# Optimization experiments

Hardware: AMD Instinct MI355X
Metric: run time of the kernel (lower is better)

## Reference

```python
import jax, jax.numpy as jnp
import numpy as np

HEAD_NUM = 8
NEG_BIG = 1e9  # additive mask constant from the original layer


def setup_inputs() -> dict:
    key = jax.random.key(0)
    ks = jax.random.split(key, 7)
    B, S, D = 4, 2048, 512
    return {
        "x": jax.random.normal(ks[0], (B, S, D), dtype=jnp.float32),
        "Wk": jax.random.normal(ks[1], (D, D), dtype=jnp.float32) * (1.0 / np.sqrt(D)),
        "bk": jax.random.normal(ks[2], (D,), dtype=jnp.float32) * 0.02,
        "Wv": jax.random.normal(ks[3], (D, D), dtype=jnp.float32) * (1.0 / np.sqrt(D)),
        "bv": jax.random.normal(ks[4], (D,), dtype=jnp.float32) * 0.02,
        "Wo": jax.random.normal(ks[5], (D, D), dtype=jnp.float32) * (1.0 / np.sqrt(D)),
        "bo": jax.random.normal(ks[6], (D,), dtype=jnp.float32) * 0.02,
    }


def reference(x, Wk, bk, Wv, bv, Wo, bo):
    B, S, D = x.shape
    H = HEAD_NUM
    hd = D // H
    # Original layer: query is NOT projected; key/value are.
    q = x
    k = x @ Wk + bk
    v = x @ Wv + bv
    # split heads: [B, H, S, hd]
    qh = q.reshape(B, S, H, hd).transpose(0, 2, 1, 3)
    kh = k.reshape(B, S, H, hd).transpose(0, 2, 1, 3)
    vh = v.reshape(B, S, H, hd).transpose(0, 2, 1, 3)
    # scaled dot-product scores [B, H, S, S] (normalized=True => 1/sqrt(head_dim))
    scale = 1.0 / jnp.sqrt(jnp.asarray(hd, dtype=x.dtype))
    e = jnp.einsum("bhqd,bhkd->bhqk", qh, kh) * scale
    # history_only=True => causal additive mask
    causal = jnp.tril(jnp.ones((S, S), dtype=x.dtype))
    e = e - (1.0 - causal) * NEG_BIG
    a = jax.nn.softmax(e, axis=-1)
    out = jnp.einsum("bhqk,bhkd->bhqd", a, vh)  # [B, H, S, hd]
    out = out.transpose(0, 2, 1, 3).reshape(B, S, D)
    return out @ Wo + bo
```

## Files before the change

### kernel.cpp

```cpp
#include <hip/hip_runtime.h>
#include <stdint.h>
#include <stddef.h>

typedef short bf16x8 __attribute__((ext_vector_type(8)));
typedef float f32x4 __attribute__((ext_vector_type(4)));
typedef int i32x4 __attribute__((ext_vector_type(4)));

#define AS1 __attribute__((address_space(1)))
#define AS3 __attribute__((address_space(3)))

#define KSCALE 0.18033688011112042f
#define MFMA16(A, B, C) __builtin_amdgcn_mfma_f32_16x16x32_bf16(A, B, C, 0, 0, 0)

__device__ __forceinline__ unsigned short f2bf(float f) {
    union { float f; uint32_t u; } v; v.f = f;
    return (unsigned short)((v.u + 0x7fffu + ((v.u >> 16) & 1u)) >> 16);
}

__global__ void cvt_f32_bf16(const float* __restrict__ in, unsigned short* __restrict__ out, int n4) {
    int i = blockIdx.x * blockDim.x + threadIdx.x;
    if (i >= n4) return;
    float4 v = reinterpret_cast<const float4*>(in)[i];
    ushort4 o;
    o.x = f2bf(v.x); o.y = f2bf(v.y); o.z = f2bf(v.z); o.w = f2bf(v.w);
    reinterpret_cast<ushort4*>(out)[i] = o;
}

__global__ void wtrans3(const float* __restrict__ Wk, const float* __restrict__ Wv,
                        const float* __restrict__ Wo,
                        unsigned short* __restrict__ WkT, unsigned short* __restrict__ WvT,
                        unsigned short* __restrict__ WoT) {
    __shared__ float tile[32][33];
    const float* W = (blockIdx.z == 0) ? Wk : (blockIdx.z == 1) ? Wv : Wo;
    unsigned short* WT = (blockIdx.z == 0) ? WkT : (blockIdx.z == 1) ? WvT : WoT;
    int bk = blockIdx.x * 32, bn = blockIdx.y * 32;
    int tx = threadIdx.x, ty = threadIdx.y;
#pragma unroll
    for (int r = 0; r < 32; r += 8)
        tile[ty + r][tx] = W[(size_t)(bk + ty + r) * 512 + bn + tx];
    __syncthreads();
#pragma unroll
    for (int r = 0; r < 32; r += 8)
        WT[(size_t)(bn + ty + r) * 512 + bk + tx] = f2bf(tile[tx][ty + r]);
}

template<int EPI>
__global__ __launch_bounds__(256, 2) void gemm64(const unsigned short* __restrict__ A,
                                                 const unsigned short* __restrict__ BT,
                                                 const float* __restrict__ bias,
                                                 void* __restrict__ outp) {
    __shared__ unsigned short lA[64 * 64];
    __shared__ unsigned short lB[128 * 64];
    const int tid = threadIdx.x;
    const int tile_n = blockIdx.x * 128;
    const int tile_m = blockIdx.y * 64;
    const int wid = tid >> 6, lane = tid & 63;
    const int wm = (wid >> 1) * 32, wn = (wid & 1) * 64;
    const int l16 = lane & 15, lg = lane >> 4;

    f32x4 acc[2][4];
#pragma unroll
    for (int i = 0; i < 2; ++i)
#pragma unroll
        for (int j = 0; j < 4; ++j)
            acc[i][j] = (f32x4){0.f, 0.f, 0.f, 0.f};

    const int r0 = tid >> 3;
    const int cr = tid & 7;

    for (int kt = 0; kt < 512; kt += 64) {
#pragma unroll
        for (int i = 0; i < 2; ++i) {
            int r = r0 + i * 32;
            int crs = cr ^ (r & 7);
            __builtin_amdgcn_global_load_lds((const AS1 void*)(A + (size_t)(tile_m + r) * 512 + kt + crs * 8),
                                             (AS3 void*)(&lA[(i * 256 + tid) * 8]), 16, 0, 0);
        }
#pragma unroll
        for (int i = 0; i < 4; ++i) {
            int r = r0 + i * 32;
            int crs = cr ^ (r & 7);
            __builtin_amdgcn_global_load_lds((const AS1 void*)(BT + (size_t)(tile_n + r) * 512 + kt + crs * 8),
                                             (AS3 void*)(&lB[(i * 256 + tid) * 8]), 16, 0, 0);
        }
        __syncthreads();
#pragma unroll
        for (int ks = 0; ks < 2; ++ks) {
            bf16x8 af[2], bfr[4];
#pragma unroll
            for (int f = 0; f < 2; ++f) {
                int ra = wm + f * 16 + l16;
                af[f] = *reinterpret_cast<const bf16x8*>(
                    reinterpret_cast<const char*>(lA) + ra * 128 + (((ks * 4 + lg) ^ (ra & 7)) << 4));
            }
#pragma unroll
            for (int f = 0; f < 4; ++f) {
                int rb = wn + f * 16 + l16;
                bfr[f] = *reinterpret_cast<const bf16x8*>(
                    reinterpret_cast<const char*>(lB) + rb * 128 + (((ks * 4 + lg) ^ (rb & 7)) << 4));
            }
#pragma unroll
            for (int fm = 0; fm < 2; ++fm)
#pragma unroll
                for (int fn = 0; fn < 4; ++fn)
                    acc[fm][fn] = MFMA16(af[fm], bfr[fn], acc[fm][fn]);
        }
        __syncthreads();
    }

#pragma unroll
    for (int fm = 0; fm < 2; ++fm)
#pragma unroll
        for (int fn = 0; fn < 4; ++fn) {
            int gm0 = tile_m + wm + fm * 16 + lg * 4;
            int gn = tile_n + wn + fn * 16 + l16;
            float bs = bias[gn];
#pragma unroll
            for (int r = 0; r < 4; ++r) {
                float v = acc[fm][fn][r] + bs;
                int m = gm0 + r;
                if (EPI == 0) {
                    v *= KSCALE;
                    int b = m >> 11, s = m & 2047, h = gn >> 6, d = gn & 63;
                    ((unsigned short*)outp)[(((size_t)(b * 8 + h) * 2048 + s) << 6) + d] = f2bf(v);
                } else if (EPI == 1) {
                    int b = m >> 11, s = m & 2047, h = gn >> 6, d = gn & 63;
                    ((unsigned short*)outp)[(((size_t)(b * 8 + h) * 64 + d) << 11) + s] = f2bf(v);
                } else {
                    ((float*)outp)[(size_t)m * 512 + gn] = v;
                }
            }
        }
}

__global__ __launch_bounds__(256, 3) void attn_f(const unsigned short* __restrict__ xq,
                                                 const unsigned short* __restrict__ kg,
                                                 const unsigned short* __restrict__ vT,
                                                 unsigned short* __restrict__ ob) {
    __shared__ unsigned short lsK[3][4096];
    __shared__ unsigned short lsV[3][4096];

    const int tid = threadIdx.x;
    const int lane = tid & 63;
    const int w = tid >> 6;
    const int l16 = lane & 15, lg = lane >> 4;
    const int bh = blockIdx.x, b = bh >> 3, h = bh & 7;
    const int qblk = 31 - blockIdx.y;
    const int qlo = qblk * 64 + w * 16;
    const int q = qlo + l16;

    const unsigned short* Kb = kg + (size_t)bh * (2048 * 64);
    const unsigned short* Vb = vT + (size_t)bh * (64 * 2048);

    const unsigned short* qp = xq + ((size_t)(b * 2048 + qlo + l16) * 512) + h * 64 + lg * 8;
    bf16x8 qf0 = *(const bf16x8*)qp;
    bf16x8 qf1 = *(const bf16x8*)(qp + 32);

    f32x4 o[4];
#pragma unroll
    for (int i = 0; i < 4; ++i) o[i] = (f32x4){0.f, 0.f, 0.f, 0.f};
    float lsum = 0.f;

    const int nph = qblk + 1;

    const int srow = tid >> 3;
    const int scs = (tid & 7) ^ (srow & 7);
    const int skey = 8 * ((srow >> 2) & 3) + (srow & 3) + 4 * (srow >> 4);

#define STAGE(B, PH) { \
        const int kv0_ = (PH) << 6; \
        __builtin_amdgcn_global_load_lds((const AS1 void*)(Kb + (size_t)(kv0_ + skey) * 64 + scs * 8), \
            (AS3 void*)(&lsK[B][(size_t)tid * 8]), 16, 0, 0); \
        __builtin_amdgcn_global_load_lds((const AS1 void*)(Kb + (size_t)(kv0_ + 32 + skey) * 64 + scs * 8), \
            (AS3 void*)(&lsK[B][(size_t)(256 + tid) * 8]), 16, 0, 0); \
        __builtin_amdgcn_global_load_lds((const AS1 void*)(Vb + (size_t)srow * 2048 + kv0_ + scs * 8), \
            (AS3 void*)(&lsV[B][(size_t)tid * 8]), 16, 0, 0); \
        __builtin_amdgcn_global_load_lds((const AS1 void*)(Vb + (size_t)(srow + 32) * 2048 + kv0_ + scs * 8), \
            (AS3 void*)(&lsV[B][(size_t)(256 + tid) * 8]), 16, 0, 0); }

#define QKGRP(G, PA, PB, KS, KVB) { \
            const char* r0p = (KS) + (32 * (G) + l16) * 128; \
            const char* r1p = r0p + 16 * 128; \
            bf16x8 k00 = *(const bf16x8*)(r0p + ((lg ^ sw) << 4)); \
            bf16x8 k01 = *(const bf16x8*)(r0p + (((lg + 4) ^ sw) << 4)); \
            bf16x8 k10 = *(const bf16x8*)(r1p + ((lg ^ sw) << 4)); \
            bf16x8 k11 = *(const bf16x8*)(r1p + (((lg + 4) ^ sw) << 4)); \
            f32x4 sA = (f32x4){0.f,0.f,0.f,0.f}, sB = (f32x4){0.f,0.f,0.f,0.f}; \
            __builtin_amdgcn_s_setprio(1); \
            sA = MFMA16(k00, qf0, sA); \
            sA = MFMA16(k01, qf1, sA); \
            sB = MFMA16(k10, qf0, sB); \
            sB = MFMA16(k11, qf1, sB); \
            __builtin_amdgcn_s_setprio(0); \
            if ((KVB) + 32 * (G) + 31 > qlo) { \
                _Pragma("unroll") \
                for (int r = 0; r < 4; ++r) { \
                    int kidx = (KVB) + 32 * (G) + 8 * lg + r; \
                    PA[r] = __builtin_amdgcn_exp2f(kidx > q ? -1e30f : sA[r]); \
                    PB[r] = __builtin_amdgcn_exp2f(kidx + 4 > q ? -1e30f : sB[r]); \
                } \
            } else { \
                _Pragma("unroll") \
                for (int r = 0; r < 4; ++r) { \
                    PA[r] = __builtin_amdgcn_exp2f(sA[r]); \
                    PB[r] = __builtin_amdgcn_exp2f(sB[r]); \
                } \
            } }

    const int sw = l16 & 7;
    STAGE(0, 0);
    if (nph > 1) STAGE(1, 1);
    int cur = 0, st = 2;
    for (int ph = 0; ph < nph; ++ph) {
        if (ph + 2 < nph) {
            STAGE(st, ph + 2);
            asm volatile("s_waitcnt vmcnt(8)" ::: "memory");
        } else if (ph + 1 < nph) {
            asm volatile("s_waitcnt vmcnt(4)" ::: "memory");
        } else {
            asm volatile("s_waitcnt vmcnt(0)" ::: "memory");
        }
        __builtin_amdgcn_s_barrier();
        asm volatile("" ::: "memory");
        {
            const char* KS = (const char*)lsK[cur];
            const char* VS = (const char*)lsV[cur];
            const int kvb = ph << 6;
            float pA0[4], pB0[4], pA1[4], pB1[4];
            QKGRP(0, pA0, pB0, KS, kvb)
            QKGRP(1, pA1, pB1, KS, kvb)
            lsum += ((pA0[0] + pA0[1]) + (pA0[2] + pA0[3]))
                  + ((pB0[0] + pB0[1]) + (pB0[2] + pB0[3]))
                  + ((pA1[0] + pA1[1]) + (pA1[2] + pA1[3]))
                  + ((pB1[0] + pB1[1]) + (pB1[2] + pB1[3]));
            uint32_t u0, u1, u2, u3, u4, u5, u6, u7;
            asm("v_cvt_pk_bf16_f32 %0, %1, %2" : "=v"(u0) : "v"(pA0[0]), "v"(pA0[1]));
            asm("v_cvt_pk_bf16_f32 %0, %1, %2" : "=v"(u1) : "v"(pA0[2]), "v"(pA0[3]));
            asm("v_cvt_pk_bf16_f32 %0, %1, %2" : "=v"(u2) : "v"(pB0[0]), "v"(pB0[1]));
            asm("v_cvt_pk_bf16_f32 %0, %1, %2" : "=v"(u3) : "v"(pB0[2]), "v"(pB0[3]));
            asm("v_cvt_pk_bf16_f32 %0, %1, %2" : "=v"(u4) : "v"(pA1[0]), "v"(pA1[1]));
            asm("v_cvt_pk_bf16_f32 %0, %1, %2" : "=v"(u5) : "v"(pA1[2]), "v"(pA1[3]));
            asm("v_cvt_pk_bf16_f32 %0, %1, %2" : "=v"(u6) : "v"(pB1[0]), "v"(pB1[1]));
            asm("v_cvt_pk_bf16_f32 %0, %1, %2" : "=v"(u7) : "v"(pB1[2]), "v"(pB1[3]));
            union { i32x4 i; bf16x8 h; } pu0, pu1;
            pu0.i = (i32x4){(int)u0, (int)u1, (int)u2, (int)u3};
            pu1.i = (i32x4){(int)u4, (int)u5, (int)u6, (int)u7};
            __builtin_amdgcn_s_setprio(1);
#pragma unroll
            for (int nb = 0; nb < 4; ++nb) {
                const char* vr = VS + (nb * 16 + l16) * 128;
                bf16x8 vf0 = *(const bf16x8*)(vr + ((lg ^ sw) << 4));
                bf16x8 vf1 = *(const bf16x8*)(vr + (((lg + 4) ^ sw) << 4));
                o[nb] = MFMA16(pu0.h, vf0, o[nb]);
                o[nb] = MFMA16(pu1.h, vf1, o[nb]);
            }
            __builtin_amdgcn_s_setprio(0);
        }
        asm volatile("" ::: "memory");
        __builtin_amdgcn_s_barrier();
        cur = (cur == 2) ? 0 : cur + 1;
        st = (st == 2) ? 0 : st + 1;
    }
#undef STAGE
#undef QKGRP

    lsum += __shfl_xor(lsum, 16, 64);
    lsum += __shfl_xor(lsum, 32, 64);
    float linv[4];
#pragma unroll
    for (int r = 0; r < 4; ++r)
        linv[r] = 1.f / __shfl(lsum, 4 * lg + r, 64);
#pragma unroll
    for (int nb = 0; nb < 4; ++nb)
#pragma unroll
        for (int r = 0; r < 4; ++r) {
            int s = qlo + 4 * lg + r;
            ob[(size_t)(b * 2048 + s) * 512 + h * 64 + nb * 16 + l16] = f2bf(o[nb][r] * linv[r]);
        }
}

extern "C" void kernel_launch(void* const* d_in, const int* in_sizes, int n_in,
                              void* d_out, int out_size, void* d_ws, size_t ws_size,
                              hipStream_t stream) {
    const float* x  = (const float*)d_in[0];
    const float* Wk = (const float*)d_in[1];
    const float* bk = (const float*)d_in[2];
    const float* Wv = (const float*)d_in[3];
    const float* bv = (const float*)d_in[4];
    const float* Wo = (const float*)d_in[5];
    const float* bo = (const float*)d_in[6];

    char* ws = (char*)d_ws;
    unsigned short* xb   = (unsigned short*)(ws);
    unsigned short* kbuf = (unsigned short*)(ws + (8ull << 20));
    unsigned short* vTb  = (unsigned short*)(ws + (16ull << 20));
    unsigned short* obuf = (unsigned short*)(ws + (24ull << 20));
    unsigned short* WkT  = (unsigned short*)(ws + (32ull << 20));
    unsigned short* WvT  = (unsigned short*)(ws + (33ull << 20));
    unsigned short* WoT  = (unsigned short*)(ws + (34ull << 20));

    cvt_f32_bf16<<<4096, 256, 0, stream>>>(x, xb, 1048576);
    wtrans3<<<dim3(16, 16, 3), dim3(32, 8), 0, stream>>>(Wk, Wv, Wo, WkT, WvT, WoT);

    dim3 gg(4, 128);
    gemm64<0><<<gg, 256, 0, stream>>>(xb, WkT, bk, kbuf);
    gemm64<1><<<gg, 256, 0, stream>>>(xb, WvT, bv, vTb);

    attn_f<<<dim3(32, 32), 256, 0, stream>>>(xb, kbuf, vTb, obuf);

    gemm64<2><<<gg, 256, 0, stream>>>(obuf, WoT, bo, (float*)d_out);
}
```

Before: 78.35 us.

## Merge prep kernels and fuse K and V projections into one GEMM launch

```diff
diff --git a/kernel.cpp b/kernel.cpp
--- a/kernel.cpp
+++ b/kernel.cpp
@@ -17,38 +17,42 @@
     return (unsigned short)((v.u + 0x7fffu + ((v.u >> 16) & 1u)) >> 16);
 }
 
-__global__ void cvt_f32_bf16(const float* __restrict__ in, unsigned short* __restrict__ out, int n4) {
-    int i = blockIdx.x * blockDim.x + threadIdx.x;
-    if (i >= n4) return;
-    float4 v = reinterpret_cast<const float4*>(in)[i];
-    ushort4 o;
-    o.x = f2bf(v.x); o.y = f2bf(v.y); o.z = f2bf(v.z); o.w = f2bf(v.w);
-    reinterpret_cast<ushort4*>(out)[i] = o;
-}
-
-__global__ void wtrans3(const float* __restrict__ Wk, const float* __restrict__ Wv,
-                        const float* __restrict__ Wo,
-                        unsigned short* __restrict__ WkT, unsigned short* __restrict__ WvT,
-                        unsigned short* __restrict__ WoT) {
+__global__ void prep(const float* __restrict__ x, const float* __restrict__ Wk,
+                     const float* __restrict__ Wv, const float* __restrict__ Wo,
+                     unsigned short* __restrict__ xb, unsigned short* __restrict__ WkvT,
+                     unsigned short* __restrict__ WoT) {
     __shared__ float tile[32][33];
-    const float* W = (blockIdx.z == 0) ? Wk : (blockIdx.z == 1) ? Wv : Wo;
-    unsigned short* WT = (blockIdx.z == 0) ? WkT : (blockIdx.z == 1) ? WvT : WoT;
-    int bk = blockIdx.x * 32, bn = blockIdx.y * 32;
-    int tx = threadIdx.x, ty = threadIdx.y;
-#pragma unroll
-    for (int r = 0; r < 32; r += 8)
-        tile[ty + r][tx] = W[(size_t)(bk + ty + r) * 512 + bn + tx];
-    __syncthreads();
-#pragma unroll
-    for (int r = 0; r < 32; r += 8)
-        WT[(size_t)(bn + ty + r) * 512 + bk + tx] = f2bf(tile[tx][ty + r]);
-}
-
-template<int EPI>
-__global__ __launch_bounds__(256, 2) void gemm64(const unsigned short* __restrict__ A,
+    const int bi = blockIdx.x;
+    const int tid = threadIdx.x;
+    if (bi < 4096) {
+        int i = bi * 256 + tid;
+        float4 v = reinterpret_cast<const float4*>(x)[i];
+        ushort4 o;
+        o.x = f2bf(v.x); o.y = f2bf(v.y); o.z = f2bf(v.z); o.w = f2bf(v.w);
+        reinterpret_cast<ushort4*>(xb)[i] = o;
+    } else {
+        int j = bi - 4096;
+        int z = j >> 8, rem = j & 255;
+        int bk = (rem >> 4) * 32, bn = (rem & 15) * 32;
+        const float* W = (z == 0) ? Wk : (z == 1) ? Wv : Wo;
+        unsigned short* WT = (z == 2) ? WoT : (WkvT + (size_t)z * 512 * 512);
+        int tx = tid & 31, ty = tid >> 5;
+#pragma unroll
+        for (int r = 0; r < 32; r += 8)
+            tile[ty + r][tx] = W[(size_t)(bk + ty + r) * 512 + bn + tx];
+        __syncthreads();
+#pragma unroll
+        for (int r = 0; r < 32; r += 8)
+            WT[(size_t)(bn + ty + r) * 512 + bk + tx] = f2bf(tile[tx][ty + r]);
+    }
+}
+
+__global__ __launch_bounds__(256, 2) void gemmKV(const unsigned short* __restrict__ A,
                                                  const unsigned short* __restrict__ BT,
-                                                 const float* __restrict__ bias,
-                                                 void* __restrict__ outp) {
+                                                 const float* __restrict__ bk,
+                                                 const float* __restrict__ bv,
+                                                 unsigned short* __restrict__ kbuf,
+                                                 unsigned short* __restrict__ vTb) {
     __shared__ unsigned short lA[64 * 64];
     __shared__ unsigned short lB[128 * 64];
     const int tid = threadIdx.x;
@@ -114,22 +118,96 @@
         for (int fn = 0; fn < 4; ++fn) {
             int gm0 = tile_m + wm + fm * 16 + lg * 4;
             int gn = tile_n + wn + fn * 16 + l16;
-            float bs = bias[gn];
+            bool isK = gn < 512;
+            int gnn = isK ? gn : gn - 512;
+            float bs = isK ? bk[gnn] : bv[gnn];
+            int hh = gnn >> 6, d = gnn & 63;
 #pragma unroll
             for (int r = 0; r < 4; ++r) {
                 float v = acc[fm][fn][r] + bs;
                 int m = gm0 + r;
-                if (EPI == 0) {
-                    v *= KSCALE;
-                    int b = m >> 11, s = m & 2047, h = gn >> 6, d = gn & 63;
-                    ((unsigned short*)outp)[(((size_t)(b * 8 + h) * 2048 + s) << 6) + d] = f2bf(v);
-                } else if (EPI == 1) {
-                    int b = m >> 11, s = m & 2047, h = gn >> 6, d = gn & 63;
-                    ((unsigned short*)outp)[(((size_t)(b * 8 + h) * 64 + d) << 11) + s] = f2bf(v);
-                } else {
-                    ((float*)outp)[(size_t)m * 512 + gn] = v;
-                }
-            }
+                int b = m >> 11, s = m & 2047;
+                if (isK)
+                    kbuf[(((size_t)(b * 8 + hh) * 2048 + s) << 6) + d] = f2bf(v * KSCALE);
+                else
+                    vTb[(((size_t)(b * 8 + hh) * 64 + d) << 11) + s] = f2bf(v);
+            }
+        }
+}
+
+__global__ __launch_bounds__(256, 2) void gemmO(const unsigned short* __restrict__ A,
+                                                const unsigned short* __restrict__ BT,
+                                                const float* __restrict__ bias,
+                                                float* __restrict__ outp) {
+    __shared__ unsigned short lA[64 * 64];
+    __shared__ unsigned short lB[128 * 64];
+    const int tid = threadIdx.x;
+    const int tile_n = blockIdx.x * 128;
+    const int tile_m = blockIdx.y * 64;
+    const int wid = tid >> 6, lane = tid & 63;
+    const int wm = (wid >> 1) * 32, wn = (wid & 1) * 64;
+    const int l16 = lane & 15, lg = lane >> 4;
+
+    f32x4 acc[2][4];
+#pragma unroll
+    for (int i = 0; i < 2; ++i)
+#pragma unroll
+        for (int j = 0; j < 4; ++j)
+            acc[i][j] = (f32x4){0.f, 0.f, 0.f, 0.f};
+
+    const int r0 = tid >> 3;
+    const int cr = tid & 7;
+
+    for (int kt = 0; kt < 512; kt += 64) {
+#pragma unroll
+        for (int i = 0; i < 2; ++i) {
+            int r = r0 + i * 32;
+            int crs = cr ^ (r & 7);
+            __builtin_amdgcn_global_load_lds((const AS1 void*)(A + (size_t)(tile_m + r) * 512 + kt + crs * 8),
+                                             (AS3 void*)(&lA[(i * 256 + tid) * 8]), 16, 0, 0);
+        }
+#pragma unroll
+        for (int i = 0; i < 4; ++i) {
+            int r = r0 + i * 32;
+            int crs = cr ^ (r & 7);
+            __builtin_amdgcn_global_load_lds((const AS1 void*)(BT + (size_t)(tile_n + r) * 512 + kt + crs * 8),
+                                             (AS3 void*)(&lB[(i * 256 + tid) * 8]), 16, 0, 0);
+        }
+        __syncthreads();
+#pragma unroll
+        for (int ks = 0; ks < 2; ++ks) {
+            bf16x8 af[2], bfr[4];
+#pragma unroll
+            for (int f = 0; f < 2; ++f) {
+                int ra = wm + f * 16 + l16;
+                af[f] = *reinterpret_cast<const bf16x8*>(
+                    reinterpret_cast<const char*>(lA) + ra * 128 + (((ks * 4 + lg) ^ (ra & 7)) << 4));
+            }
+#pragma unroll
+            for (int f = 0; f < 4; ++f) {
+                int rb = wn + f * 16 + l16;
+                bfr[f] = *reinterpret_cast<const bf16x8*>(
+                    reinterpret_cast<const char*>(lB) + rb * 128 + (((ks * 4 + lg) ^ (rb & 7)) << 4));
+            }
+#pragma unroll
+            for (int fm = 0; fm < 2; ++fm)
+#pragma unroll
+                for (int fn = 0; fn < 4; ++fn)
+                    acc[fm][fn] = MFMA16(af[fm], bfr[fn], acc[fm][fn]);
+        }
+        __syncthreads();
+    }
+
+#pragma unroll
+    for (int fm = 0; fm < 2; ++fm)
+#pragma unroll
+        for (int fn = 0; fn < 4; ++fn) {
+            int gm0 = tile_m + wm + fm * 16 + lg * 4;
+            int gn = tile_n + wn + fn * 16 + l16;
+            float bs = bias[gn];
+#pragma unroll
+            for (int r = 0; r < 4; ++r)
+                outp[(size_t)(gm0 + r) * 512 + gn] = acc[fm][fn][r] + bs;
         }
 }
 
@@ -291,22 +369,18 @@
     const float* bo = (const float*)d_in[6];
 
     char* ws = (char*)d_ws;
-    unsigned short* xb   = (unsigned short*)(ws);
-    unsigned short* kbuf = (unsigned short*)(ws + (8ull << 20));
-    unsigned short* vTb  = (unsigned short*)(ws + (16ull << 20));
-    unsigned short* obuf = (unsigned short*)(ws + (24ull << 20));
-    unsigned short* WkT  = (unsigned short*)(ws + (32ull << 20));
-    unsigned short* WvT  = (unsigned short*)(ws + (33ull << 20));
-    unsigned short* WoT  = (unsigned short*)(ws + (34ull << 20));
-
-    cvt_f32_bf16<<<4096, 256, 0, stream>>>(x, xb, 1048576);
-    wtrans3<<<dim3(16, 16, 3), dim3(32, 8), 0, stream>>>(Wk, Wv, Wo, WkT, WvT, WoT);
-
-    dim3 gg(4, 128);
-    gemm64<0><<<gg, 256, 0, stream>>>(xb, WkT, bk, kbuf);
-    gemm64<1><<<gg, 256, 0, stream>>>(xb, WvT, bv, vTb);
+    unsigned short* xb    = (unsigned short*)(ws);
+    unsigned short* kbuf  = (unsigned short*)(ws + (8ull << 20));
+    unsigned short* vTb   = (unsigned short*)(ws + (16ull << 20));
+    unsigned short* obuf  = (unsigned short*)(ws + (24ull << 20));
+    unsigned short* WkvT  = (unsigned short*)(ws + (32ull << 20));
+    unsigned short* WoT   = (unsigned short*)(ws + (33ull << 20));
+
+    prep<<<4864, 256, 0, stream>>>(x, Wk, Wv, Wo, xb, WkvT, WoT);
+
+    gemmKV<<<dim3(8, 128), 256, 0, stream>>>(xb, WkvT, bk, bv, kbuf, vTb);
 
     attn_f<<<dim3(32, 32), 256, 0, stream>>>(xb, kbuf, vTb, obuf);
 
-    gemm64<2><<<gg, 256, 0, stream>>>(obuf, WoT, bo, (float*)d_out);
-}
+    gemmO<<<dim3(4, 128), 256, 0, stream>>>(obuf, WoT, bo, (float*)d_out);
+}
```

New measurement: 85.07 us. 8.6% more time.
